# Kernel tuning notes

Hardware: AMD Instinct MI355X
Metric: run time of the kernel (lower is better)

Reference implementation:

```python
import jax, jax.numpy as jnp
import numpy as np
import math

N_HEADS = 16

def _rope_tables(T, D, dtype):
    # inv_freq over even dims, emb = [freqs, freqs] -> [T, D]
    inv_freq = 1.0 / (10000.0 ** (jnp.arange(0, D, 2, dtype=jnp.float32) / D))
    freqs = jnp.arange(T, dtype=jnp.float32)[:, None] * inv_freq[None, :]  # [T, D/2]
    emb = jnp.concatenate([freqs, freqs], axis=-1)  # [T, D]
    return jnp.cos(emb).astype(dtype), jnp.sin(emb).astype(dtype)

def _rotate_half(x):
    d = x.shape[-1] // 2
    return jnp.concatenate([-x[..., d:], x[..., :d]], axis=-1)

def setup_inputs() -> dict:
    key = jax.random.key(0)
    ks = jax.random.split(key, 5)
    B, T, C = 2, 2048, 1024
    s = 1.0 / math.sqrt(C)
    return {
        "x": jax.random.normal(ks[0], (B, T, C), dtype=jnp.float32),
        "Wq": jax.random.normal(ks[1], (C, C), dtype=jnp.float32) * s,
        "Wk": jax.random.normal(ks[2], (C, C), dtype=jnp.float32) * s,
        "Wv": jax.random.normal(ks[3], (C, C), dtype=jnp.float32) * s,
        "Wo": jax.random.normal(ks[4], (C, C), dtype=jnp.float32) * s,
    }

def reference(x, Wq, Wk, Wv, Wo):
    B, T, C = x.shape
    H = N_HEADS
    D = C // H
    # QKV projections (torch Linear, bias=False: y = x @ W.T), split into heads
    def proj(W):
        return (x @ W.T).reshape(B, T, H, D).transpose(0, 2, 1, 3)  # [B,H,T,D]
    q, k, v = proj(Wq), proj(Wk), proj(Wv)
    # RoPE
    cos, sin = _rope_tables(T, D, x.dtype)  # [T,D] each, broadcast over B,H
    q = q * cos + _rotate_half(q) * sin
    k = k * cos + _rotate_half(k) * sin
    # scaled dot-product attention with causal mask
    scale = 1.0 / math.sqrt(D)
    attn = jnp.einsum('bhtd,bhsd->bhts', q, k) * scale  # [B,H,T,T]
    row = jnp.arange(T)[:, None]
    col = jnp.arange(T)[None, :]
    attn = jnp.where(col > row, -jnp.inf, attn)
    p = jax.nn.softmax(attn, axis=-1)
    out = jnp.einsum('bhts,bhsd->bhtd', p, v)  # [B,H,T,D]
    out = out.transpose(0, 2, 1, 3).reshape(B, T, C)
    return out @ Wo.T
```

## Files before the change

kernel.cpp:

```cpp
#include <hip/hip_runtime.h>
#include <hip/hip_bf16.h>


typedef __hip_bfloat16 bf16;
typedef __attribute__((ext_vector_type(8))) short bf16x8;
typedef __attribute__((ext_vector_type(4))) float f32x4;
typedef __attribute__((ext_vector_type(4))) short short4v;

#define MFMA16(a, b, c) __builtin_amdgcn_mfma_f32_16x16x32_bf16((a), (b), (c), 0, 0, 0)

constexpr int Bn = 2, Hn = 16, Tn = 2048, Dn = 64, Cn = 1024;
constexpr size_t NE = (size_t)Bn * Tn * Cn;
constexpr size_t WE = (size_t)Cn * Cn;
constexpr float QSCALE = 0.125f * 1.44269504088896f;

__device__ inline unsigned short bfbits(float x) {
    bf16 b = __float2bfloat16(x);
    return *(unsigned short*)&b;
}

__device__ inline bf16x8 pack8(f32x4 a, f32x4 b) {
    bf16x8 r;
#pragma unroll
    for (int i = 0; i < 4; ++i) r[i] = (short)bfbits(a[i]);
#pragma unroll
    for (int i = 0; i < 4; ++i) r[4 + i] = (short)bfbits(b[i]);
    return r;
}

__device__ inline void gl_lds16(const bf16* g, unsigned short* l) {
    __builtin_amdgcn_global_load_lds(
        (const __attribute__((address_space(1))) void*)g,
        (__attribute__((address_space(3))) void*)l, 16, 0, 0);
}

__global__ __launch_bounds__(256) void convert_kernel(
    const float* __restrict__ x, const float* __restrict__ wq,
    const float* __restrict__ wk, const float* __restrict__ wv,
    const float* __restrict__ wo, bf16* __restrict__ dst)
{
    int blk = blockIdx.x;
    int lane = threadIdx.x & 63;
    int lx = lane & 15, quad = lane >> 4;
    const float* src;
    size_t doff;
    if (blk < 2048) {
        int frag = blk * 4 + (threadIdx.x >> 6);
        int mt = frag >> 5, kc = frag & 31;
        src = x + (size_t)(mt * 16 + lx) * Cn + kc * 32 + quad * 8;
        doff = (size_t)frag * 512 + lane * 8;
    } else {
        int w = (blk - 2048) >> 9, b = (blk - 2048) & 511;
        const float* s4[4] = {wq, wk, wv, wo};
        int frag = b * 4 + (threadIdx.x >> 6);
        int nb = frag >> 5, kc = frag & 31;
        src = s4[w] + (size_t)(nb * 16 + lx) * Cn + kc * 32 + quad * 8;
        doff = NE + (size_t)w * WE + (size_t)frag * 512 + lane * 8;
    }
    f32x4 a = *(const f32x4*)(src);
    f32x4 b2 = *(const f32x4*)(src + 4);
    *(bf16x8*)(dst + doff) = pack8(a, b2);
}

__global__ __launch_bounds__(256) void gemm_qkv_kernel(
    const bf16* __restrict__ Xf, const bf16* __restrict__ Wbase,
    bf16* __restrict__ Qo, bf16* __restrict__ Ko, bf16* __restrict__ Vo)
{
    const int bm = blockIdx.x, bn = blockIdx.y, wsel = blockIdx.z;
    const bf16* W = Wbase + (size_t)wsel * WE;
    const int tid  = threadIdx.x;
    const int wave = tid >> 6, lane = tid & 63;
    const int lx   = lane & 15, quad = lane >> 4;
    const int wm = wave >> 1, wn = wave & 1;

    const int mt0 = bm * 8 + wm * 4;
    const int nb0 = bn * 8 + wn * 4;
    const bf16* afrag = Xf + (size_t)mt0 * 32 * 512 + (size_t)lane * 8;
    const bf16* wfrag = W + (size_t)nb0 * 32 * 512 + (size_t)lane * 8;

    f32x4 acc[4][4] = {};
    bf16x8 acur[4], bcur[4], anxt[4], bnxt[4];
#pragma unroll
    for (int i = 0; i < 4; ++i) {
        acur[i] = *(const bf16x8*)(afrag + (size_t)i * 32 * 512);
        bcur[i] = *(const bf16x8*)(wfrag + (size_t)i * 32 * 512);
    }
    for (int kc = 0; kc < 32; ++kc) {
        if (kc < 31) {
#pragma unroll
            for (int i = 0; i < 4; ++i) {
                anxt[i] = *(const bf16x8*)(afrag + ((size_t)i * 32 + kc + 1) * 512);
                bnxt[i] = *(const bf16x8*)(wfrag + ((size_t)i * 32 + kc + 1) * 512);
            }
        }
#pragma unroll
        for (int mt = 0; mt < 4; ++mt)
#pragma unroll
            for (int nt = 0; nt < 4; ++nt)
                acc[mt][nt] = MFMA16(acur[mt], bcur[nt], acc[mt][nt]);
#pragma unroll
        for (int i = 0; i < 4; ++i) { acur[i] = anxt[i]; bcur[i] = bnxt[i]; }
    }

    const int h = bn * 2 + wn;
    if (wsel <= 1) {
#pragma unroll
        for (int mt = 0; mt < 4; ++mt)
#pragma unroll
            for (int r = 0; r < 4; ++r) {
                int mg = bm * 128 + wm * 64 + mt * 16 + quad * 4 + r;
                int t  = mg & (Tn - 1);
#pragma unroll
                for (int nt = 0; nt < 2; ++nt) {
                    int d = nt * 16 + lx;
                    float ang = (float)t * __expf(-(float)d * 0.2878231366f);
                    float c, s;
                    __sincosf(ang, &s, &c);
                    float a0 = acc[mt][nt][r], a1 = acc[mt][nt + 2][r];
                    acc[mt][nt][r]     = a0 * c - a1 * s;
                    acc[mt][nt + 2][r] = a1 * c + a0 * s;
                }
            }
    }

#pragma unroll
    for (int mt = 0; mt < 4; ++mt) {
        int mg0 = bm * 128 + wm * 64 + mt * 16 + quad * 4;
        int b = mg0 >> 11, tlo = mg0 & (Tn - 1);
        if (wsel == 0) {
#pragma unroll
            for (int nt = 0; nt < 4; ++nt)
#pragma unroll
                for (int r = 0; r < 4; ++r) {
                    int d = nt * 16 + lx;
                    Qo[((size_t)(b * Hn + h) * Tn + tlo + r) * Dn + d] =
                        __float2bfloat16(acc[mt][nt][r] * QSCALE);
                }
        } else if (wsel == 1) {
            bf16* Kf = Ko + (size_t)(b * Hn + h) * Tn * Dn;
            int c = tlo >> 6, ntk = (tlo >> 4) & 3;
#pragma unroll
            for (int nt = 0; nt < 4; ++nt) {
                size_t base = ((size_t)(c * 4 + ntk) * 2 + (nt >> 1)) * 512
                            + (size_t)((nt & 1) * 2 + (lx >> 3)) * 128
                            + (size_t)(tlo & 15) * 8 + (lx & 7);
#pragma unroll
                for (int r = 0; r < 4; ++r)
                    Kf[base + (size_t)r * 8] = __float2bfloat16(acc[mt][nt][r]);
            }
        } else {
            bf16* Vf = Vo + (size_t)(b * Hn + h) * Tn * Dn;
            int c = tlo >> 6, ksv = (tlo >> 5) & 1;
            int qv = (tlo >> 3) & 3, pos0 = tlo & 7;
#pragma unroll
            for (int nt = 0; nt < 4; ++nt) {
                short4v pk;
#pragma unroll
                for (int r = 0; r < 4; ++r) pk[r] = (short)bfbits(acc[mt][nt][r]);
                *(short4v*)&Vf[((size_t)(c * 8 + nt * 2 + ksv)) * 512
                               + (size_t)qv * 128 + (size_t)lx * 8 + pos0] = pk;
            }
        }
    }
}

__global__ __launch_bounds__(256) void gemm_out_kernel(
    const bf16* __restrict__ Af, const bf16* __restrict__ W, float* __restrict__ Out)
{
    const int bm = blockIdx.x, bn = blockIdx.y;
    const int tid  = threadIdx.x;
    const int wave = tid >> 6, lane = tid & 63;
    const int lx   = lane & 15, quad = lane >> 4;
    const int wm = wave >> 1, wn = wave & 1;

    const int mt0 = bm * 8 + wm * 4;
    const int nb0 = bn * 4 + wn * 2;
    const bf16* afrag = Af + (size_t)mt0 * 32 * 512 + (size_t)lane * 8;
    const bf16* wfrag = W + (size_t)nb0 * 32 * 512 + (size_t)lane * 8;

    f32x4 acc[4][2] = {};
    bf16x8 acur[4], bcur[2], anxt[4], bnxt[2];
#pragma unroll
    for (int i = 0; i < 4; ++i)
        acur[i] = *(const bf16x8*)(afrag + (size_t)i * 32 * 512);
#pragma unroll
    for (int i = 0; i < 2; ++i)
        bcur[i] = *(const bf16x8*)(wfrag + (size_t)i * 32 * 512);
    for (int kc = 0; kc < 32; ++kc) {
        if (kc < 31) {
#pragma unroll
            for (int i = 0; i < 4; ++i)
                anxt[i] = *(const bf16x8*)(afrag + ((size_t)i * 32 + kc + 1) * 512);
#pragma unroll
            for (int i = 0; i < 2; ++i)
                bnxt[i] = *(const bf16x8*)(wfrag + ((size_t)i * 32 + kc + 1) * 512);
        }
#pragma unroll
        for (int mt = 0; mt < 4; ++mt)
#pragma unroll
            for (int nt = 0; nt < 2; ++nt)
                acc[mt][nt] = MFMA16(acur[mt], bcur[nt], acc[mt][nt]);
#pragma unroll
        for (int i = 0; i < 4; ++i) acur[i] = anxt[i];
#pragma unroll
        for (int i = 0; i < 2; ++i) bcur[i] = bnxt[i];
    }
#pragma unroll
    for (int mt = 0; mt < 4; ++mt)
#pragma unroll
        for (int nt = 0; nt < 2; ++nt)
#pragma unroll
            for (int r = 0; r < 4; ++r) {
                int mg = bm * 128 + wm * 64 + mt * 16 + quad * 4 + r;
                int ng = bn * 64 + wn * 32 + nt * 16 + lx;
                Out[(size_t)mg * Cn + ng] = acc[mt][nt][r];
            }
}

__global__ __launch_bounds__(256) void attn_kernel(
    const bf16* __restrict__ Q, const bf16* __restrict__ K,
    const bf16* __restrict__ Vt, bf16* __restrict__ O)
{
    __shared__ unsigned short Ks[4096];
    __shared__ unsigned short Vs[4096];
    __shared__ unsigned short Pl[4][16 * 72];
    const int f  = blockIdx.x;
    const int bh = (f & 7) * 4 + ((f >> 3) & 3);
    const int qb = 31 - (f >> 5);
    const int tid  = threadIdx.x;
    const int wave = tid >> 6, lane = tid & 63;
    const int lx   = lane & 15, quad = lane >> 4;

    const bf16* Qh = Q  + (size_t)bh * Tn * Dn;
    const bf16* Kh = K  + (size_t)bh * Tn * Dn;
    const bf16* Vh = Vt + (size_t)bh * Tn * Dn;
    unsigned short* pw = &Pl[wave][0];

    const int qrowA = qb * 64 + wave * 16 + lx;
    bf16x8 aq0 = *(const bf16x8*)(Qh + (size_t)qrowA * Dn + quad * 8);
    bf16x8 aq1 = *(const bf16x8*)(Qh + (size_t)qrowA * Dn + 32 + quad * 8);

    bf16x8 ones;
#pragma unroll
    for (int i = 0; i < 8; ++i) ones[i] = (short)0x3F80;

    f32x4 acc_o[4] = {};
    f32x4 acc_l = {};
    const int row_local = wave * 16 + quad * 4;

    for (int c = 0; c <= qb; ++c) {
        __syncthreads();
#pragma unroll
        for (int j = 0; j < 2; ++j) {
            int base = (j * 256 + wave * 64) * 8;
            gl_lds16(Kh + (size_t)c * 4096 + base + lane * 8, Ks + base);
            gl_lds16(Vh + (size_t)c * 4096 + base + lane * 8, Vs + base);
        }
        __syncthreads();
        f32x4 accs[4] = {};
#pragma unroll
        for (int nt = 0; nt < 4; ++nt) {
            bf16x8 k0 = *(const bf16x8*)&Ks[(nt * 2) * 512 + lane * 8];
            bf16x8 k1 = *(const bf16x8*)&Ks[(nt * 2 + 1) * 512 + lane * 8];
            accs[nt] = MFMA16(aq0, k0, accs[nt]);
            accs[nt] = MFMA16(aq1, k1, accs[nt]);
        }
        if (c < qb) {
#pragma unroll
            for (int nt = 0; nt < 4; ++nt)
#pragma unroll
                for (int r = 0; r < 4; ++r)
                    pw[(quad * 4 + r) * 72 + nt * 16 + lx] = bfbits(exp2f(accs[nt][r]));
        } else {
#pragma unroll
            for (int nt = 0; nt < 4; ++nt) {
                int keyl = nt * 16 + lx;
#pragma unroll
                for (int r = 0; r < 4; ++r) {
                    float p = (keyl > row_local + r) ? 0.0f : exp2f(accs[nt][r]);
                    pw[(quad * 4 + r) * 72 + nt * 16 + lx] = bfbits(p);
                }
            }
        }
        asm volatile("s_waitcnt lgkmcnt(0)" ::: "memory");
        bf16x8 ap0 = *(const bf16x8*)&pw[lx * 72 + quad * 8];
        bf16x8 ap1 = *(const bf16x8*)&pw[lx * 72 + 32 + quad * 8];
        acc_l = MFMA16(ap0, ones, acc_l);
        acc_l = MFMA16(ap1, ones, acc_l);
#pragma unroll
        for (int dt = 0; dt < 4; ++dt) {
            bf16x8 v0 = *(const bf16x8*)&Vs[(dt * 2) * 512 + lane * 8];
            bf16x8 v1 = *(const bf16x8*)&Vs[(dt * 2 + 1) * 512 + lane * 8];
            acc_o[dt] = MFMA16(ap0, v0, acc_o[dt]);
            acc_o[dt] = MFMA16(ap1, v1, acc_o[dt]);
        }
    }

    const int b = bh >> 4, h = bh & 15;
    const int mtile = b * 128 + qb * 4 + wave;
#pragma unroll
    for (int dt = 0; dt < 4; ++dt) {
        int ch = h * 64 + dt * 16 + lx;
        size_t base = ((size_t)mtile * 32 + (ch >> 5)) * 512
                    + (size_t)(((ch >> 3) & 3) * 16) * 8 + (ch & 7);
#pragma unroll
        for (int r = 0; r < 4; ++r) {
            float o = acc_o[dt][r] / acc_l[r];
            O[base + (size_t)(quad * 4 + r) * 8] = __float2bfloat16(o);
        }
    }
}

extern "C" void kernel_launch(void* const* d_in, const int* in_sizes, int n_in,
                              void* d_out, int out_size, void* d_ws, size_t ws_size,
                              hipStream_t stream)
{
    const float* x  = (const float*)d_in[0];
    const float* Wq = (const float*)d_in[1];
    const float* Wk = (const float*)d_in[2];
    const float* Wv = (const float*)d_in[3];
    const float* Wo = (const float*)d_in[4];
    float* out = (float*)d_out;

    bf16* ws = (bf16*)d_ws;
    bf16* Xf = ws;
    bf16* Wb = ws + NE;
    bf16* Qb = ws + NE + 4 * WE;
    bf16* Kb = Qb + NE;
    bf16* Vb = Kb + NE;
    bf16* Ab = Xf;

    convert_kernel<<<4096, 256, 0, stream>>>(x, Wq, Wk, Wv, Wo, ws);
    gemm_qkv_kernel<<<dim3(32, 8, 3), 256, 0, stream>>>(Xf, Wb, Qb, Kb, Vb);
    attn_kernel<<<1024, 256, 0, stream>>>(Qb, Kb, Vb, Ab);
    gemm_out_kernel<<<dim3(32, 16), 256, 0, stream>>>(Ab, Wb + 3 * WE, out);
}
```

Before: 177.2 us.

## Stage GEMM tiles through double-buffered LDS with direct global-to-LDS loads

Both projection GEMMs now stage their A and W fragments in double-buffered shared memory using direct global-to-LDS loads. Each fragment is fetched once per block and shared by all four waves, where before each wave reloaded its own fragments from global memory. Block indices are remapped so neighbouring blocks land on the same XCD-style group, and the output GEMM tile widens to 128x128. The cost is a barrier every k step and half as many blocks for the output GEMM, which lowers parallelism.

```diff
diff --git a/kernel.cpp b/kernel.cpp
--- a/kernel.cpp
+++ b/kernel.cpp
@@ -66,40 +66,63 @@
     const bf16* __restrict__ Xf, const bf16* __restrict__ Wbase,
     bf16* __restrict__ Qo, bf16* __restrict__ Ko, bf16* __restrict__ Vo)
 {
-    const int bm = blockIdx.x, bn = blockIdx.y, wsel = blockIdx.z;
+    __shared__ unsigned short sm[2][16 * 512];
+
+    const int linear = blockIdx.x;
+    const int wid = (linear & 7) * 96 + (linear >> 3);
+    const int wsel = wid >> 8;
+    const int rem  = wid & 255;
+    const int bm = rem >> 3, bn = rem & 7;
+
     const bf16* W = Wbase + (size_t)wsel * WE;
     const int tid  = threadIdx.x;
     const int wave = tid >> 6, lane = tid & 63;
     const int lx   = lane & 15, quad = lane >> 4;
     const int wm = wave >> 1, wn = wave & 1;
 
-    const int mt0 = bm * 8 + wm * 4;
-    const int nb0 = bn * 8 + wn * 4;
-    const bf16* afrag = Xf + (size_t)mt0 * 32 * 512 + (size_t)lane * 8;
-    const bf16* wfrag = W + (size_t)nb0 * 32 * 512 + (size_t)lane * 8;
+    const bf16* src[4];
+#pragma unroll
+    for (int i = 0; i < 4; ++i) {
+        int frag = wave * 4 + i;
+        src[i] = (frag < 8)
+            ? Xf + (size_t)(bm * 8 + frag) * 32 * 512 + lane * 8
+            : W  + (size_t)(bn * 8 + frag - 8) * 32 * 512 + lane * 8;
+    }
+    unsigned short* dst0 = &sm[0][(wave * 4) * 512];
+    unsigned short* dst1 = &sm[1][(wave * 4) * 512];
+    const unsigned short* ra0 = &sm[0][(wm * 4) * 512 + lane * 8];
+    const unsigned short* rb0 = &sm[0][(8 + wn * 4) * 512 + lane * 8];
+    const unsigned short* ra1 = &sm[1][(wm * 4) * 512 + lane * 8];
+    const unsigned short* rb1 = &sm[1][(8 + wn * 4) * 512 + lane * 8];
 
     f32x4 acc[4][4] = {};
-    bf16x8 acur[4], bcur[4], anxt[4], bnxt[4];
-#pragma unroll
-    for (int i = 0; i < 4; ++i) {
-        acur[i] = *(const bf16x8*)(afrag + (size_t)i * 32 * 512);
-        bcur[i] = *(const bf16x8*)(wfrag + (size_t)i * 32 * 512);
-    }
+
+#pragma unroll
+    for (int i = 0; i < 4; ++i)
+        gl_lds16(src[i], dst0 + i * 512);
+    __syncthreads();
+
     for (int kc = 0; kc < 32; ++kc) {
         if (kc < 31) {
-#pragma unroll
-            for (int i = 0; i < 4; ++i) {
-                anxt[i] = *(const bf16x8*)(afrag + ((size_t)i * 32 + kc + 1) * 512);
-                bnxt[i] = *(const bf16x8*)(wfrag + ((size_t)i * 32 + kc + 1) * 512);
-            }
+            unsigned short* dn = (kc & 1) ? dst0 : dst1;
+#pragma unroll
+            for (int i = 0; i < 4; ++i)
+                gl_lds16(src[i] + (size_t)(kc + 1) * 512, dn + i * 512);
+        }
+        const unsigned short* ra = (kc & 1) ? ra1 : ra0;
+        const unsigned short* rb = (kc & 1) ? rb1 : rb0;
+        bf16x8 av[4], bv[4];
+#pragma unroll
+        for (int j = 0; j < 4; ++j) {
+            av[j] = *(const bf16x8*)(ra + j * 512);
+            bv[j] = *(const bf16x8*)(rb + j * 512);
         }
 #pragma unroll
         for (int mt = 0; mt < 4; ++mt)
 #pragma unroll
             for (int nt = 0; nt < 4; ++nt)
-                acc[mt][nt] = MFMA16(acur[mt], bcur[nt], acc[mt][nt]);
-#pragma unroll
-        for (int i = 0; i < 4; ++i) { acur[i] = anxt[i]; bcur[i] = bnxt[i]; }
+                acc[mt][nt] = MFMA16(av[mt], bv[nt], acc[mt][nt]);
+        __syncthreads();
     }
 
     const int h = bn * 2 + wn;
@@ -167,52 +190,70 @@
 __global__ __launch_bounds__(256) void gemm_out_kernel(
     const bf16* __restrict__ Af, const bf16* __restrict__ W, float* __restrict__ Out)
 {
-    const int bm = blockIdx.x, bn = blockIdx.y;
+    __shared__ unsigned short sm[2][16 * 512];
+
+    const int linear = blockIdx.x;
+    const int wid = (linear & 7) * 32 + (linear >> 3);
+    const int bm = wid >> 3, bn = wid & 7;
+
     const int tid  = threadIdx.x;
     const int wave = tid >> 6, lane = tid & 63;
     const int lx   = lane & 15, quad = lane >> 4;
     const int wm = wave >> 1, wn = wave & 1;
 
-    const int mt0 = bm * 8 + wm * 4;
-    const int nb0 = bn * 4 + wn * 2;
-    const bf16* afrag = Af + (size_t)mt0 * 32 * 512 + (size_t)lane * 8;
-    const bf16* wfrag = W + (size_t)nb0 * 32 * 512 + (size_t)lane * 8;
-
-    f32x4 acc[4][2] = {};
-    bf16x8 acur[4], bcur[2], anxt[4], bnxt[2];
+    const bf16* src[4];
+#pragma unroll
+    for (int i = 0; i < 4; ++i) {
+        int frag = wave * 4 + i;
+        src[i] = (frag < 8)
+            ? Af + (size_t)(bm * 8 + frag) * 32 * 512 + lane * 8
+            : W  + (size_t)(bn * 8 + frag - 8) * 32 * 512 + lane * 8;
+    }
+    unsigned short* dst0 = &sm[0][(wave * 4) * 512];
+    unsigned short* dst1 = &sm[1][(wave * 4) * 512];
+    const unsigned short* ra0 = &sm[0][(wm * 4) * 512 + lane * 8];
+    const unsigned short* rb0 = &sm[0][(8 + wn * 4) * 512 + lane * 8];
+    const unsigned short* ra1 = &sm[1][(wm * 4) * 512 + lane * 8];
+    const unsigned short* rb1 = &sm[1][(8 + wn * 4) * 512 + lane * 8];
+
+    f32x4 acc[4][4] = {};
+
 #pragma unroll
     for (int i = 0; i < 4; ++i)
-        acur[i] = *(const bf16x8*)(afrag + (size_t)i * 32 * 512);
-#pragma unroll
-    for (int i = 0; i < 2; ++i)
-        bcur[i] = *(const bf16x8*)(wfrag + (size_t)i * 32 * 512);
+        gl_lds16(src[i], dst0 + i * 512);
+    __syncthreads();
+
     for (int kc = 0; kc < 32; ++kc) {
         if (kc < 31) {
+            unsigned short* dn = (kc & 1) ? dst0 : dst1;
 #pragma unroll
             for (int i = 0; i < 4; ++i)
-                anxt[i] = *(const bf16x8*)(afrag + ((size_t)i * 32 + kc + 1) * 512);
-#pragma unroll
-            for (int i = 0; i < 2; ++i)
-                bnxt[i] = *(const bf16x8*)(wfrag + ((size_t)i * 32 + kc + 1) * 512);
+                gl_lds16(src[i] + (size_t)(kc + 1) * 512, dn + i * 512);
+        }
+        const unsigned short* ra = (kc & 1) ? ra1 : ra0;
+        const unsigned short* rb = (kc & 1) ? rb1 : rb0;
+        bf16x8 av[4], bv[4];
+#pragma unroll
+        for (int j = 0; j < 4; ++j) {
+            av[j] = *(const bf16x8*)(ra + j * 512);
+            bv[j] = *(const bf16x8*)(rb + j * 512);
         }
 #pragma unroll
         for (int mt = 0; mt < 4; ++mt)
 #pragma unroll
-            for (int nt = 0; nt < 2; ++nt)
-                acc[mt][nt] = MFMA16(acur[mt], bcur[nt], acc[mt][nt]);
-#pragma unroll
-        for (int i = 0; i < 4; ++i) acur[i] = anxt[i];
-#pragma unroll
-        for (int i = 0; i < 2; ++i) bcur[i] = bnxt[i];
-    }
+            for (int nt = 0; nt < 4; ++nt)
+                acc[mt][nt] = MFMA16(av[mt], bv[nt], acc[mt][nt]);
+        __syncthreads();
+    }
+
 #pragma unroll
     for (int mt = 0; mt < 4; ++mt)
 #pragma unroll
-        for (int nt = 0; nt < 2; ++nt)
+        for (int nt = 0; nt < 4; ++nt)
 #pragma unroll
             for (int r = 0; r < 4; ++r) {
                 int mg = bm * 128 + wm * 64 + mt * 16 + quad * 4 + r;
-                int ng = bn * 64 + wn * 32 + nt * 16 + lx;
+                int ng = bn * 128 + wn * 64 + nt * 16 + lx;
                 Out[(size_t)mg * Cn + ng] = acc[mt][nt][r];
             }
 }
@@ -331,7 +372,7 @@
     bf16* Ab = Xf;
 
     convert_kernel<<<4096, 256, 0, stream>>>(x, Wq, Wk, Wv, Wo, ws);
-    gemm_qkv_kernel<<<dim3(32, 8, 3), 256, 0, stream>>>(Xf, Wb, Qb, Kb, Vb);
+    gemm_qkv_kernel<<<768, 256, 0, stream>>>(Xf, Wb, Qb, Kb, Vb);
     attn_kernel<<<1024, 256, 0, stream>>>(Qb, Kb, Vb, Ab);
-    gemm_out_kernel<<<dim3(32, 16), 256, 0, stream>>>(Ab, Wb + 3 * WE, out);
-}
+    gemm_out_kernel<<<256, 256, 0, stream>>>(Ab, Wb + 3 * WE, out);
+}
```

After: 185.8 us. 4.8% more time.

## Double-buffer K/V tiles in attention with async prefetch and MFMA priority

Applied to the files above, without the earlier changes.

The attention kernel now keeps two LDS buffers for K and V and prefetches the next key block while the current one is computed. Explicit vmcnt waits and raw barriers replace the two __syncthreads per iteration. s_setprio raises wave priority around the MFMA sections, and the P staging stride changes from 72 to 68 to alter the LDS bank mapping. This doubles K/V LDS usage, which may lower occupancy, and relies on hand-counted vmcnt values being correct.

```diff
diff --git a/kernel.cpp b/kernel.cpp
--- a/kernel.cpp
+++ b/kernel.cpp
@@ -13,6 +13,7 @@
 constexpr size_t NE = (size_t)Bn * Tn * Cn;
 constexpr size_t WE = (size_t)Cn * Cn;
 constexpr float QSCALE = 0.125f * 1.44269504088896f;
+constexpr int PS = 68;
 
 __device__ inline unsigned short bfbits(float x) {
     bf16 b = __float2bfloat16(x);
@@ -221,9 +222,9 @@
     const bf16* __restrict__ Q, const bf16* __restrict__ K,
     const bf16* __restrict__ Vt, bf16* __restrict__ O)
 {
-    __shared__ unsigned short Ks[4096];
-    __shared__ unsigned short Vs[4096];
-    __shared__ unsigned short Pl[4][16 * 72];
+    __shared__ unsigned short Ks[2][4096];
+    __shared__ unsigned short Vs[2][4096];
+    __shared__ unsigned short Pl[4][16 * PS];
     const int f  = blockIdx.x;
     const int bh = (f & 7) * 4 + ((f >> 3) & 3);
     const int qb = 31 - (f >> 5);
@@ -247,30 +248,46 @@
     f32x4 acc_o[4] = {};
     f32x4 acc_l = {};
     const int row_local = wave * 16 + quad * 4;
+    const int sbase = wave * 64 * 8;
+
+#pragma unroll
+    for (int j = 0; j < 2; ++j) {
+        int base = j * 256 * 8 + sbase;
+        gl_lds16(Kh + base + lane * 8, &Ks[0][base]);
+        gl_lds16(Vh + base + lane * 8, &Vs[0][base]);
+    }
 
     for (int c = 0; c <= qb; ++c) {
-        __syncthreads();
-#pragma unroll
-        for (int j = 0; j < 2; ++j) {
-            int base = (j * 256 + wave * 64) * 8;
-            gl_lds16(Kh + (size_t)c * 4096 + base + lane * 8, Ks + base);
-            gl_lds16(Vh + (size_t)c * 4096 + base + lane * 8, Vs + base);
-        }
-        __syncthreads();
+        const int pb = c & 1;
+        if (c < qb) {
+#pragma unroll
+            for (int j = 0; j < 2; ++j) {
+                int base = j * 256 * 8 + sbase;
+                gl_lds16(Kh + (size_t)(c + 1) * 4096 + base + lane * 8, &Ks[pb ^ 1][base]);
+                gl_lds16(Vh + (size_t)(c + 1) * 4096 + base + lane * 8, &Vs[pb ^ 1][base]);
+            }
+            asm volatile("s_waitcnt vmcnt(4)" ::: "memory");
+        } else {
+            asm volatile("s_waitcnt vmcnt(0)" ::: "memory");
+        }
+        asm volatile("s_barrier" ::: "memory");
+
         f32x4 accs[4] = {};
+        __builtin_amdgcn_s_setprio(1);
 #pragma unroll
         for (int nt = 0; nt < 4; ++nt) {
-            bf16x8 k0 = *(const bf16x8*)&Ks[(nt * 2) * 512 + lane * 8];
-            bf16x8 k1 = *(const bf16x8*)&Ks[(nt * 2 + 1) * 512 + lane * 8];
+            bf16x8 k0 = *(const bf16x8*)&Ks[pb][(nt * 2) * 512 + lane * 8];
+            bf16x8 k1 = *(const bf16x8*)&Ks[pb][(nt * 2 + 1) * 512 + lane * 8];
             accs[nt] = MFMA16(aq0, k0, accs[nt]);
             accs[nt] = MFMA16(aq1, k1, accs[nt]);
         }
+        __builtin_amdgcn_s_setprio(0);
         if (c < qb) {
 #pragma unroll
             for (int nt = 0; nt < 4; ++nt)
 #pragma unroll
                 for (int r = 0; r < 4; ++r)
-                    pw[(quad * 4 + r) * 72 + nt * 16 + lx] = bfbits(exp2f(accs[nt][r]));
+                    pw[(quad * 4 + r) * PS + nt * 16 + lx] = bfbits(exp2f(accs[nt][r]));
         } else {
 #pragma unroll
             for (int nt = 0; nt < 4; ++nt) {
@@ -278,22 +295,25 @@
 #pragma unroll
                 for (int r = 0; r < 4; ++r) {
                     float p = (keyl > row_local + r) ? 0.0f : exp2f(accs[nt][r]);
-                    pw[(quad * 4 + r) * 72 + nt * 16 + lx] = bfbits(p);
+                    pw[(quad * 4 + r) * PS + nt * 16 + lx] = bfbits(p);
                 }
             }
         }
         asm volatile("s_waitcnt lgkmcnt(0)" ::: "memory");
-        bf16x8 ap0 = *(const bf16x8*)&pw[lx * 72 + quad * 8];
-        bf16x8 ap1 = *(const bf16x8*)&pw[lx * 72 + 32 + quad * 8];
+        bf16x8 ap0 = *(const bf16x8*)&pw[lx * PS + quad * 8];
+        bf16x8 ap1 = *(const bf16x8*)&pw[lx * PS + 32 + quad * 8];
+        __builtin_amdgcn_s_setprio(1);
         acc_l = MFMA16(ap0, ones, acc_l);
         acc_l = MFMA16(ap1, ones, acc_l);
 #pragma unroll
         for (int dt = 0; dt < 4; ++dt) {
-            bf16x8 v0 = *(const bf16x8*)&Vs[(dt * 2) * 512 + lane * 8];
-            bf16x8 v1 = *(const bf16x8*)&Vs[(dt * 2 + 1) * 512 + lane * 8];
+            bf16x8 v0 = *(const bf16x8*)&Vs[pb][(dt * 2) * 512 + lane * 8];
+            bf16x8 v1 = *(const bf16x8*)&Vs[pb][(dt * 2 + 1) * 512 + lane * 8];
             acc_o[dt] = MFMA16(ap0, v0, acc_o[dt]);
             acc_o[dt] = MFMA16(ap1, v1, acc_o[dt]);
         }
+        __builtin_amdgcn_s_setprio(0);
+        asm volatile("s_barrier" ::: "memory");
     }
 
     const int b = bh >> 4, h = bh & 15;
```

Result: slower. 187.4 us (+5.8%).

## Load K/V tiles directly into registers with next-K prefetch, drop LDS staging

Applied to the files above, without the earlier changes.

The attention kernel no longer stages K and V chunks through shared memory with block-wide barriers. Each wave now loads its K and V fragments straight from global memory into registers and prefetches the next chunk's K while computing the current one. This removes both __syncthreads per iteration and the LDS round trip. In exchange, each of the four waves redundantly loads the same K/V data from global/L2, register pressure rises, and the P scratch row stride changes from 72 to 68.

```diff
diff --git a/kernel.cpp b/kernel.cpp
--- a/kernel.cpp
+++ b/kernel.cpp
@@ -13,6 +13,7 @@
 constexpr size_t NE = (size_t)Bn * Tn * Cn;
 constexpr size_t WE = (size_t)Cn * Cn;
 constexpr float QSCALE = 0.125f * 1.44269504088896f;
+constexpr int PS = 68;
 
 __device__ inline unsigned short bfbits(float x) {
     bf16 b = __float2bfloat16(x);
@@ -26,12 +27,6 @@
 #pragma unroll
     for (int i = 0; i < 4; ++i) r[4 + i] = (short)bfbits(b[i]);
     return r;
-}
-
-__device__ inline void gl_lds16(const bf16* g, unsigned short* l) {
-    __builtin_amdgcn_global_load_lds(
-        (const __attribute__((address_space(1))) void*)g,
-        (__attribute__((address_space(3))) void*)l, 16, 0, 0);
 }
 
 __global__ __launch_bounds__(256) void convert_kernel(
@@ -221,9 +216,7 @@
     const bf16* __restrict__ Q, const bf16* __restrict__ K,
     const bf16* __restrict__ Vt, bf16* __restrict__ O)
 {
-    __shared__ unsigned short Ks[4096];
-    __shared__ unsigned short Vs[4096];
-    __shared__ unsigned short Pl[4][16 * 72];
+    __shared__ unsigned short Pl[4][16 * PS];
     const int f  = blockIdx.x;
     const int bh = (f & 7) * 4 + ((f >> 3) & 3);
     const int qb = 31 - (f >> 5);
@@ -248,29 +241,34 @@
     f32x4 acc_l = {};
     const int row_local = wave * 16 + quad * 4;
 
+    bf16x8 kc[8], kn[8], vc[8];
+#pragma unroll
+    for (int i = 0; i < 8; ++i)
+        kc[i] = *(const bf16x8*)(Kh + (size_t)i * 512 + lane * 8);
+
     for (int c = 0; c <= qb; ++c) {
-        __syncthreads();
-#pragma unroll
-        for (int j = 0; j < 2; ++j) {
-            int base = (j * 256 + wave * 64) * 8;
-            gl_lds16(Kh + (size_t)c * 4096 + base + lane * 8, Ks + base);
-            gl_lds16(Vh + (size_t)c * 4096 + base + lane * 8, Vs + base);
-        }
-        __syncthreads();
+        const bf16* Vc = Vh + (size_t)c * 4096 + lane * 8;
+#pragma unroll
+        for (int i = 0; i < 8; ++i)
+            vc[i] = *(const bf16x8*)(Vc + (size_t)i * 512);
+        if (c < qb) {
+            const bf16* Kc = Kh + (size_t)(c + 1) * 4096 + lane * 8;
+#pragma unroll
+            for (int i = 0; i < 8; ++i)
+                kn[i] = *(const bf16x8*)(Kc + (size_t)i * 512);
+        }
         f32x4 accs[4] = {};
 #pragma unroll
         for (int nt = 0; nt < 4; ++nt) {
-            bf16x8 k0 = *(const bf16x8*)&Ks[(nt * 2) * 512 + lane * 8];
-            bf16x8 k1 = *(const bf16x8*)&Ks[(nt * 2 + 1) * 512 + lane * 8];
-            accs[nt] = MFMA16(aq0, k0, accs[nt]);
-            accs[nt] = MFMA16(aq1, k1, accs[nt]);
+            accs[nt] = MFMA16(aq0, kc[nt * 2], accs[nt]);
+            accs[nt] = MFMA16(aq1, kc[nt * 2 + 1], accs[nt]);
         }
         if (c < qb) {
 #pragma unroll
             for (int nt = 0; nt < 4; ++nt)
 #pragma unroll
                 for (int r = 0; r < 4; ++r)
-                    pw[(quad * 4 + r) * 72 + nt * 16 + lx] = bfbits(exp2f(accs[nt][r]));
+                    pw[(quad * 4 + r) * PS + nt * 16 + lx] = bfbits(exp2f(accs[nt][r]));
         } else {
 #pragma unroll
             for (int nt = 0; nt < 4; ++nt) {
@@ -278,21 +276,23 @@
 #pragma unroll
                 for (int r = 0; r < 4; ++r) {
                     float p = (keyl > row_local + r) ? 0.0f : exp2f(accs[nt][r]);
-                    pw[(quad * 4 + r) * 72 + nt * 16 + lx] = bfbits(p);
+                    pw[(quad * 4 + r) * PS + nt * 16 + lx] = bfbits(p);
                 }
             }
         }
         asm volatile("s_waitcnt lgkmcnt(0)" ::: "memory");
-        bf16x8 ap0 = *(const bf16x8*)&pw[lx * 72 + quad * 8];
-        bf16x8 ap1 = *(const bf16x8*)&pw[lx * 72 + 32 + quad * 8];
+        bf16x8 ap0 = *(const bf16x8*)&pw[lx * PS + quad * 8];
+        bf16x8 ap1 = *(const bf16x8*)&pw[lx * PS + 32 + quad * 8];
         acc_l = MFMA16(ap0, ones, acc_l);
         acc_l = MFMA16(ap1, ones, acc_l);
 #pragma unroll
         for (int dt = 0; dt < 4; ++dt) {
-            bf16x8 v0 = *(const bf16x8*)&Vs[(dt * 2) * 512 + lane * 8];
-            bf16x8 v1 = *(const bf16x8*)&Vs[(dt * 2 + 1) * 512 + lane * 8];
-            acc_o[dt] = MFMA16(ap0, v0, acc_o[dt]);
-            acc_o[dt] = MFMA16(ap1, v1, acc_o[dt]);
+            acc_o[dt] = MFMA16(ap0, vc[dt * 2], acc_o[dt]);
+            acc_o[dt] = MFMA16(ap1, vc[dt * 2 + 1], acc_o[dt]);
+        }
+        if (c < qb) {
+#pragma unroll
+            for (int i = 0; i < 8; ++i) kc[i] = kn[i];
         }
     }
 
```

Measured after the change: 180.8 us. 2.0% more time.
